# Optimization experiments

Hardware: AMD Instinct MI355X
Metric: run time of the kernel (lower is better)

## Reference

```python
import jax, jax.numpy as jnp
import numpy as np

EPS = 1e-7
TOPK = 10
IOU_THR = 0.1
REG_W, OBJ_W, CLS_W = 5.0, 1.0, 1.0
NUM_CLASSES = 80
STRIDES = (8, 16, 32)


def _corners(b):
    cx, cy, w, h = b[..., 0], b[..., 1], b[..., 2], b[..., 3]
    return cx - w / 2, cy - h / 2, cx + w / 2, cy + h / 2


def bbox_iou(box1, box2, ciou=False):
    # boxes in (cx, cy, w, h); broadcastable shapes [..., 4]
    x11, y11, x12, y12 = _corners(box1)
    x21, y21, x22, y22 = _corners(box2)
    iw = jnp.clip(jnp.minimum(x12, x22) - jnp.maximum(x11, x21), 0)
    ih = jnp.clip(jnp.minimum(y12, y22) - jnp.maximum(y11, y21), 0)
    inter = iw * ih
    a1 = (x12 - x11) * (y12 - y11)
    a2 = (x22 - x21) * (y22 - y21)
    union = a1 + a2 - inter + EPS
    iou = inter / union
    if not ciou:
        return iou
    cw = jnp.maximum(x12, x22) - jnp.minimum(x11, x21)
    ch = jnp.maximum(y12, y22) - jnp.minimum(y11, y21)
    c2 = cw ** 2 + ch ** 2 + EPS
    rho2 = ((x21 + x22 - x11 - x12) ** 2 + (y21 + y22 - y11 - y12) ** 2) / 4
    v = 4 / 3.14159 ** 2 * (jnp.arctan((x22 - x21) / (y22 - y21 + EPS))
                            - jnp.arctan((x12 - x11) / (y12 - y11 + EPS))) ** 2
    alpha = jax.lax.stop_gradient(v / (1 - iou + v + EPS))
    return iou - (rho2 / c2 + v * alpha)


def _bce_logits(x, t):
    # BCEWithLogitsLoss, reduction='none' (numerically stable)
    return jnp.maximum(x, 0) - x * t + jnp.log1p(jnp.exp(-jnp.abs(x)))


def _flat(p):
    # [B, C, H, W] -> [B, H*W, C] matching permute(1,2,0).reshape(-1, C)
    B, C, H, W = p.shape
    return p.transpose(0, 2, 3, 1).reshape(B, H * W, C)


def _grids(shapes):
    gs, ss = [], []
    for (H, W), s in zip(shapes, STRIDES):
        yv, xv = jnp.meshgrid(jnp.arange(H), jnp.arange(W), indexing='ij')
        gs.append(jnp.stack([xv, yv], -1).astype(jnp.float32).reshape(-1, 2))
        ss.append(jnp.full((H * W,), float(s), dtype=jnp.float32))
    return jnp.concatenate(gs, 0), jnp.concatenate(ss, 0)


def _yolox_loss(p3_cls, p3_reg, p3_obj, p4_cls, p4_reg, p4_obj,
                p5_cls, p5_reg, p5_obj, targets):
    B = p3_cls.shape[0]
    shapes = [p3_cls.shape[2:], p4_cls.shape[2:], p5_cls.shape[2:]]
    grids, strides = _grids(shapes)            # [A,2], [A]
    cls_preds = jnp.concatenate([_flat(p3_cls), _flat(p4_cls), _flat(p5_cls)], 1)  # [B,A,C]
    reg_preds = jnp.concatenate([_flat(p3_reg), _flat(p4_reg), _flat(p5_reg)], 1)  # [B,A,4]
    obj_preds = jnp.concatenate([_flat(p3_obj), _flat(p4_obj), _flat(p5_obj)], 1)[..., 0]  # [B,A]
    A = cls_preds.shape[1]

    # decode predicted boxes (cx, cy, w, h) in image coords
    pred_cx = (grids[:, 0] + jax.nn.sigmoid(reg_preds[..., 0])) * strides
    pred_cy = (grids[:, 1] + jax.nn.sigmoid(reg_preds[..., 1])) * strides
    pred_w = jnp.exp(reg_preds[..., 2]) * strides
    pred_h = jnp.exp(reg_preds[..., 3]) * strides
    pred_boxes = jnp.stack([pred_cx, pred_cy, pred_w, pred_h], -1)  # [B,A,4]

    # targets: (x, y, w, h, class) with x,y top-left -> center format
    t_cx = targets[..., 0] + targets[..., 2] / 2
    t_cy = targets[..., 1] + targets[..., 3] / 2
    tboxes = jnp.stack([t_cx, t_cy, targets[..., 2], targets[..., 3]], -1)  # [B,T,4]
    tcls = targets[..., 4].astype(jnp.int32)  # [B,T]

    # SimOTA-style candidate selection: top-k closest anchor centers per target
    ac = grids * strides[:, None] + strides[:, None] / 2  # [A,2]
    dist = jnp.sqrt((ac[None, None, :, 0] - t_cx[..., None]) ** 2
                    + (ac[None, None, :, 1] - t_cy[..., None]) ** 2)  # [B,T,A]
    _, idx = jax.lax.top_k(-dist, TOPK)  # [B,T,K] smallest distances

    bidx = jnp.arange(B)[:, None, None]
    sel_boxes = pred_boxes[bidx, idx]                           # [B,T,K,4]
    ious = bbox_iou(sel_boxes, tboxes[:, :, None, :])           # [B,T,K]
    valid = ious > IOU_THR
    has_valid = valid.any(-1, keepdims=True)
    fallback = jnp.arange(TOPK) == jnp.argmax(ious, -1)[..., None]
    amask = jnp.where(has_valid, valid, fallback)               # [B,T,K] bool
    w = amask.astype(jnp.float32)
    num_pos = jnp.maximum(w.sum(), 1.0)

    cious = bbox_iou(sel_boxes, tboxes[:, :, None, :], ciou=True)
    reg_sum = ((1.0 - cious) * w).sum()

    # classification loss at assigned anchors
    sel_cls = cls_preds[bidx, idx]                              # [B,T,K,C]
    onehot = jax.nn.one_hot(tcls, NUM_CLASSES, dtype=jnp.float32)[:, :, None, :]
    cls_sum = (_bce_logits(sel_cls, onehot).sum(-1) * w).sum()

    # objectness: target 1 at any assigned anchor (scatter-max), 0 elsewhere
    obj_t = jnp.zeros((B, A), jnp.float32).at[bidx, idx].max(w)
    obj_sum = _bce_logits(obj_preds, obj_t).sum()

    reg_l = reg_sum / num_pos
    obj_l = obj_sum / num_pos
    cls_l = cls_sum / num_pos
    total = REG_W * reg_l + OBJ_W * obj_l + CLS_W * cls_l
    return jnp.stack([total, reg_l, obj_l, cls_l])


def setup_inputs() -> dict:
    key = jax.random.key(0)
    ks = jax.random.split(key, 12)
    B, T = 32, 50
    d = {}
    shapes = {'p3': (80, 80), 'p4': (40, 40), 'p5': (20, 20)}
    i = 0
    for name, (H, W) in shapes.items():
        d[f'{name}_cls'] = jax.random.normal(ks[i], (B, NUM_CLASSES, H, W), jnp.float32); i += 1
        d[f'{name}_reg'] = jax.random.normal(ks[i], (B, 4, H, W), jnp.float32); i += 1
        d[f'{name}_obj'] = jax.random.normal(ks[i], (B, 1, H, W), jnp.float32); i += 1
    xy = jax.random.uniform(ks[9], (B, T, 2)) * 500.0
    wh = jax.random.uniform(ks[10], (B, T, 2)) * 120.0 + 8.0
    cls_id = jax.random.randint(ks[11], (B, T, 1), 0, NUM_CLASSES).astype(jnp.float32)
    d['targets'] = jnp.concatenate([xy, wh, cls_id], -1)
    return d


def reference(p3_cls, p3_reg, p3_obj, p4_cls, p4_reg, p4_obj,
              p5_cls, p5_reg, p5_obj, targets):
    return _yolox_loss(p3_cls, p3_reg, p3_obj, p4_cls, p4_reg, p4_obj,
                       p5_cls, p5_reg, p5_obj, targets)
```

## Files before the change

### kernel.cpp

```cpp
#include <hip/hip_runtime.h>
#include <math.h>

#define B 32
#define T 50
#define KK 10
#define NC 80
#define A_TOT 8400
#define EPSF 1e-7f
#define IOU_THR 0.1f

#define WORDS_PER_B 264
#define BITS_BYTES (B * WORDS_PER_B * 4)

__device__ __forceinline__ float softplus_bce0(float x) {
    return fmaxf(x, 0.0f) + log1pf(expf(-fabsf(x)));
}

__device__ __forceinline__ void decode_level(int a, int& aa, int& W, int& HW, float& s) {
    if (a < 6400)      { aa = a;        W = 80; HW = 6400; s = 8.0f;  }
    else if (a < 8000) { aa = a - 6400; W = 40; HW = 1600; s = 16.0f; }
    else               { aa = a - 8000; W = 20; HW = 400;  s = 32.0f; }
}

__device__ __forceinline__ unsigned long long pack_key(float d, int id) {
    return ((unsigned long long)__float_as_uint(d) << 32) | (unsigned int)id;
}

__device__ __forceinline__ void cswk(unsigned long long& ka, unsigned long long& kb) {
    if (kb < ka) { unsigned long long t = ka; ka = kb; kb = t; }
}

__global__ __launch_bounds__(64) void fused_kernel(
    const float* __restrict__ c3, const float* __restrict__ r3,
    const float* __restrict__ c4, const float* __restrict__ r4,
    const float* __restrict__ c5, const float* __restrict__ r5,
    const float* __restrict__ o3, const float* __restrict__ o4,
    const float* __restrict__ o5, const float* __restrict__ targets,
    unsigned int* __restrict__ bits, float4* __restrict__ partials)
{
    int bt = blockIdx.x;
    int b = bt / T;
    int lane = threadIdx.x;

    int gt = bt * 64 + lane;
    float ov0 = o3[gt];
    float ov1 = o3[gt + 102400];
    float ov2 = (gt < 51200) ? o4[gt] : 0.0f;
    float ov3 = (gt < 12800) ? o5[gt] : 0.0f;

    const float* tg = targets + bt * 5;
    float tw = tg[2], th = tg[3];
    float tcx = tg[0] + tw * 0.5f, tcy = tg[1] + th * 0.5f;
    int tcls = (int)tg[4];

    int ci = lane & 7, ri = lane >> 3;

    unsigned long long k0, k1, k2;
    {
        int j0 = (int)(tcx * 0.125f), i0 = (int)(tcy * 0.125f);
        int js = min(max(j0 - 3, 0), 72), is = min(max(i0 - 3, 0), 72);
        int j = js + ci, i = is + ri;
        float dx = j * 8.0f + 4.0f - tcx, dy = i * 8.0f + 4.0f - tcy;
        k0 = pack_key(sqrtf(dx * dx + dy * dy), i * 80 + j);
    }
    {
        int j0 = (int)(tcx * 0.0625f), i0 = (int)(tcy * 0.0625f);
        int js = min(max(j0 - 3, 0), 32), is = min(max(i0 - 3, 0), 32);
        int j = js + ci, i = is + ri;
        float dx = j * 16.0f + 8.0f - tcx, dy = i * 16.0f + 8.0f - tcy;
        k1 = pack_key(sqrtf(dx * dx + dy * dy), 6400 + i * 40 + j);
    }
    {
        int j0 = (int)(tcx * 0.03125f), i0 = (int)(tcy * 0.03125f);
        int js = min(max(j0 - 3, 0), 12), is = min(max(i0 - 3, 0), 12);
        int j = js + ci, i = is + ri;
        float dx = j * 32.0f + 16.0f - tcx, dy = i * 32.0f + 16.0f - tcy;
        k2 = pack_key(sqrtf(dx * dx + dy * dy), 8000 + i * 20 + j);
    }
    cswk(k0, k1); cswk(k1, k2); cswk(k0, k1);

    int a = 0;
    for (int k = 0; k < KK; ++k) {
        unsigned long long bk = k0;
#pragma unroll
        for (int sft = 1; sft < 64; sft <<= 1) {
            unsigned long long ok = __shfl_xor(bk, sft);
            if (ok < bk) bk = ok;
        }
        if (k0 == bk) {
            k0 = k1; k1 = k2; k2 = ~0ull;
        }
        if (lane == k) a = (int)(unsigned int)(bk & 0xffffffffull);
    }

    float x21 = tcx - tw * 0.5f, y21 = tcy - th * 0.5f;
    float x22 = tcx + tw * 0.5f, y22 = tcy + th * 0.5f;

    float iou = -INFINITY, ciou = 0.0f;
    bool valid = false;
    if (lane < KK) {
        int aa, W, HW; float s;
        decode_level(a, aa, W, HW, s);
        int i = aa / W, j = aa - i * W;
        const float* rb = (HW == 6400) ? r3 : (HW == 1600 ? r4 : r5);
        size_t rbase = ((size_t)b * 4) * (size_t)HW + (size_t)aa;
        float r0 = rb[rbase];
        float r1 = rb[rbase + (size_t)HW];
        float r2 = rb[rbase + 2 * (size_t)HW];
        float r3v = rb[rbase + 3 * (size_t)HW];
        float px = ((float)j + 1.0f / (1.0f + expf(-r0))) * s;
        float py = ((float)i + 1.0f / (1.0f + expf(-r1))) * s;
        float pw = expf(r2) * s;
        float ph = expf(r3v) * s;
        float x11 = px - pw * 0.5f, y11 = py - ph * 0.5f;
        float x12 = px + pw * 0.5f, y12 = py + ph * 0.5f;
        float iw = fmaxf(fminf(x12, x22) - fmaxf(x11, x21), 0.0f);
        float ih = fmaxf(fminf(y12, y22) - fmaxf(y11, y21), 0.0f);
        float inter = iw * ih;
        float a1 = (x12 - x11) * (y12 - y11);
        float a2 = (x22 - x21) * (y22 - y21);
        float uni = a1 + a2 - inter + EPSF;
        iou = inter / uni;
        valid = iou > IOU_THR;
        float cw = fmaxf(x12, x22) - fminf(x11, x21);
        float ch = fmaxf(y12, y22) - fminf(y11, y21);
        float c2 = cw * cw + ch * ch + EPSF;
        float ddx = x21 + x22 - x11 - x12;
        float ddy = y21 + y22 - y11 - y12;
        float rho2 = (ddx * ddx + ddy * ddy) * 0.25f;
        const float CPI = (float)(4.0 / (3.14159 * 3.14159));
        float dat = atanf((x22 - x21) / (y22 - y21 + EPSF))
                  - atanf((x12 - x11) / (y12 - y11 + EPSF));
        float v = CPI * dat * dat;
        float alpha = v / (1.0f - iou + v + EPSF);
        ciou = iou - (rho2 / c2 + v * alpha);
    }

    unsigned long long vmask = __ballot(valid);
    bool has_valid = (vmask != 0ull);

    float bi = iou; int bl = lane;
#pragma unroll
    for (int sft = 1; sft < 64; sft <<= 1) {
        float oi = __shfl_xor(bi, sft);
        int ol  = __shfl_xor(bl, sft);
        if (oi > bi || (oi == bi && ol < bl)) { bi = oi; bl = ol; }
    }

    bool w = (lane < KK) && (has_valid ? valid : (lane == bl));
    unsigned long long wmask0 = __ballot(w);
    int nw = __popcll(wmask0);

    float regc = w ? (1.0f - ciou) : 0.0f;
#pragma unroll
    for (int sft = 1; sft < 64; sft <<= 1) regc += __shfl_xor(regc, sft);

    unsigned int oldbits = 0, bit = 0;
    if (w) {
        bit = 1u << (a & 31);
        oldbits = atomicOr(&bits[b * WORDS_PER_B + (a >> 5)], bit);
    }

    __shared__ int s_aid[16];
    if (w) {
        int rank = __popcll(wmask0 & ((1ull << lane) - 1ull));
        s_aid[rank] = a;
    }
    __syncthreads();
    int n_items = nw * NC;

    auto cls_ptr = [&](int item, int& c) -> const float* {
        int k = item / NC;
        c = item - k * NC;
        int ak = s_aid[k];
        int aak, Wk, HWk; float sk;
        decode_level(ak, aak, Wk, HWk, sk);
        const float* cb = (HWk == 6400) ? c3 : (HWk == 1600 ? c4 : c5);
        return cb + ((size_t)b * NC + (size_t)c) * (size_t)HWk + (size_t)aak;
    };

    bool m0 = lane < n_items;
    bool m1 = 64 + lane < n_items;
    bool m2 = 128 + lane < n_items;
    bool m3 = 192 + lane < n_items;
    int cc0 = 0, cc1 = 0, cc2 = 0, cc3 = 0;
    float v0 = 0.0f, v1 = 0.0f, v2 = 0.0f, v3 = 0.0f;
    if (m0) v0 = *cls_ptr(lane, cc0);
    if (m1) v1 = *cls_ptr(64 + lane, cc1);
    if (m2) v2 = *cls_ptr(128 + lane, cc2);
    if (m3) v3 = *cls_ptr(192 + lane, cc3);

    float osum = softplus_bce0(ov0) + softplus_bce0(ov1);
    if (gt < 51200) osum += softplus_bce0(ov2);
    if (gt < 12800) osum += softplus_bce0(ov3);
    if (w && !(oldbits & bit)) {
        int aa, W, HW; float s;
        decode_level(a, aa, W, HW, s);
        const float* ob = (HW == 6400) ? o3 : (HW == 1600 ? o4 : o5);
        osum -= ob[(size_t)b * HW + aa];
    }
#pragma unroll
    for (int sft = 1; sft < 64; sft <<= 1) osum += __shfl_xor(osum, sft);

    float csum = 0.0f;
    if (m0) csum += softplus_bce0(v0) - (cc0 == tcls ? v0 : 0.0f);
    if (m1) csum += softplus_bce0(v1) - (cc1 == tcls ? v1 : 0.0f);
    if (m2) csum += softplus_bce0(v2) - (cc2 == tcls ? v2 : 0.0f);
    if (m3) csum += softplus_bce0(v3) - (cc3 == tcls ? v3 : 0.0f);
    for (int base = 256; base < n_items; base += 64) {
        int item = base + lane;
        if (item < n_items) {
            int c;
            float v = *cls_ptr(item, c);
            csum += softplus_bce0(v) - (c == tcls ? v : 0.0f);
        }
    }
#pragma unroll
    for (int sft = 1; sft < 64; sft <<= 1) csum += __shfl_xor(csum, sft);

    if (lane == 0)
        partials[bt] = make_float4(regc, csum, (float)nw, osum);
}

__global__ __launch_bounds__(256) void finalize_kernel(
    const float4* __restrict__ partials, float* __restrict__ out)
{
    int tid = threadIdx.x;
    float reg = 0.0f, cls = 0.0f, np = 0.0f, obj = 0.0f;
    for (int i = tid; i < B * T; i += 256) {
        float4 p = partials[i];
        reg += p.x; cls += p.y; np += p.z; obj += p.w;
    }
#pragma unroll
    for (int sft = 1; sft < 64; sft <<= 1) {
        reg += __shfl_xor(reg, sft);
        cls += __shfl_xor(cls, sft);
        np  += __shfl_xor(np, sft);
        obj += __shfl_xor(obj, sft);
    }
    __shared__ float sred[4][4];
    int wv = tid >> 6;
    if ((tid & 63) == 0) {
        sred[wv][0] = reg; sred[wv][1] = cls; sred[wv][2] = np; sred[wv][3] = obj;
    }
    __syncthreads();
    if (tid == 0) {
        float R = 0, C = 0, N = 0, O = 0;
        for (int i = 0; i < 4; ++i) {
            R += sred[i][0]; C += sred[i][1]; N += sred[i][2]; O += sred[i][3];
        }
        float npf = fmaxf(N, 1.0f);
        float reg_l = R / npf, cls_l = C / npf, obj_l = O / npf;
        out[0] = 5.0f * reg_l + obj_l + cls_l;
        out[1] = reg_l;
        out[2] = obj_l;
        out[3] = cls_l;
    }
}

extern "C" void kernel_launch(void* const* d_in, const int* in_sizes, int n_in,
                              void* d_out, int out_size, void* d_ws, size_t ws_size,
                              hipStream_t stream) {
    const float* p3c = (const float*)d_in[0];
    const float* p3r = (const float*)d_in[1];
    const float* p3o = (const float*)d_in[2];
    const float* p4c = (const float*)d_in[3];
    const float* p4r = (const float*)d_in[4];
    const float* p4o = (const float*)d_in[5];
    const float* p5c = (const float*)d_in[6];
    const float* p5r = (const float*)d_in[7];
    const float* p5o = (const float*)d_in[8];
    const float* targets = (const float*)d_in[9];

    char* ws = (char*)d_ws;
    unsigned int* bits = (unsigned int*)ws;
    float4* partials = (float4*)(ws + BITS_BYTES);

    hipMemsetAsync(bits, 0, BITS_BYTES, stream);

    fused_kernel<<<B * T, 64, 0, stream>>>(p3c, p3r, p4c, p4r, p5c, p5r,
                                           p3o, p4o, p5o, targets,
                                           bits, partials);
    finalize_kernel<<<1, 256, 0, stream>>>(partials, (float*)d_out);
}
```

Measured before the change: 133.5 us.

## Fuse finalize into main kernel via last-block ticket; use fast exp/log

Removes the separate finalize kernel launch: each block publishes its partial sums with release stores and bumps an atomic ticket, and the last block to arrive reduces all partials and writes the output. The ticket is zeroed by the existing memset, which now covers it. Also swaps expf/log1pf for the __expf/__logf intrinsics and moves the objectness load for each assigned anchor earlier, next to the regression loads, so its latency overlaps. This saves one kernel launch and gap at the cost of slight precision loss from the intrinsics and a serialized tail reduction done by one wave.

```diff
diff --git a/kernel.cpp b/kernel.cpp
--- a/kernel.cpp
+++ b/kernel.cpp
@@ -11,9 +11,10 @@
 
 #define WORDS_PER_B 264
 #define BITS_BYTES (B * WORDS_PER_B * 4)
+#define ZERO_BYTES (16 + BITS_BYTES)
 
 __device__ __forceinline__ float softplus_bce0(float x) {
-    return fmaxf(x, 0.0f) + log1pf(expf(-fabsf(x)));
+    return fmaxf(x, 0.0f) + __logf(1.0f + __expf(-fabsf(x)));
 }
 
 __device__ __forceinline__ void decode_level(int a, int& aa, int& W, int& HW, float& s) {
@@ -36,7 +37,8 @@
     const float* __restrict__ c5, const float* __restrict__ r5,
     const float* __restrict__ o3, const float* __restrict__ o4,
     const float* __restrict__ o5, const float* __restrict__ targets,
-    unsigned int* __restrict__ bits, float4* __restrict__ partials)
+    unsigned int* __restrict__ ticket, unsigned int* __restrict__ bits,
+    float* __restrict__ partials, float* __restrict__ out)
 {
     int bt = blockIdx.x;
     int b = bt / T;
@@ -96,22 +98,24 @@
     float x21 = tcx - tw * 0.5f, y21 = tcy - th * 0.5f;
     float x22 = tcx + tw * 0.5f, y22 = tcy + th * 0.5f;
 
-    float iou = -INFINITY, ciou = 0.0f;
+    float iou = -INFINITY, ciou = 0.0f, ospec = 0.0f;
     bool valid = false;
     if (lane < KK) {
         int aa, W, HW; float s;
         decode_level(a, aa, W, HW, s);
         int i = aa / W, j = aa - i * W;
         const float* rb = (HW == 6400) ? r3 : (HW == 1600 ? r4 : r5);
+        const float* ob = (HW == 6400) ? o3 : (HW == 1600 ? o4 : o5);
         size_t rbase = ((size_t)b * 4) * (size_t)HW + (size_t)aa;
         float r0 = rb[rbase];
         float r1 = rb[rbase + (size_t)HW];
         float r2 = rb[rbase + 2 * (size_t)HW];
         float r3v = rb[rbase + 3 * (size_t)HW];
-        float px = ((float)j + 1.0f / (1.0f + expf(-r0))) * s;
-        float py = ((float)i + 1.0f / (1.0f + expf(-r1))) * s;
-        float pw = expf(r2) * s;
-        float ph = expf(r3v) * s;
+        ospec = ob[(size_t)b * HW + aa];
+        float px = ((float)j + 1.0f / (1.0f + __expf(-r0))) * s;
+        float py = ((float)i + 1.0f / (1.0f + __expf(-r1))) * s;
+        float pw = __expf(r2) * s;
+        float ph = __expf(r3v) * s;
         float x11 = px - pw * 0.5f, y11 = py - ph * 0.5f;
         float x12 = px + pw * 0.5f, y12 = py + ph * 0.5f;
         float iw = fmaxf(fminf(x12, x22) - fmaxf(x11, x21), 0.0f);
@@ -193,12 +197,7 @@
     float osum = softplus_bce0(ov0) + softplus_bce0(ov1);
     if (gt < 51200) osum += softplus_bce0(ov2);
     if (gt < 12800) osum += softplus_bce0(ov3);
-    if (w && !(oldbits & bit)) {
-        int aa, W, HW; float s;
-        decode_level(a, aa, W, HW, s);
-        const float* ob = (HW == 6400) ? o3 : (HW == 1600 ? o4 : o5);
-        osum -= ob[(size_t)b * HW + aa];
-    }
+    if (w && !(oldbits & bit)) osum -= ospec;
 #pragma unroll
     for (int sft = 1; sft < 64; sft <<= 1) osum += __shfl_xor(osum, sft);
 
@@ -218,43 +217,40 @@
 #pragma unroll
     for (int sft = 1; sft < 64; sft <<= 1) csum += __shfl_xor(csum, sft);
 
-    if (lane == 0)
-        partials[bt] = make_float4(regc, csum, (float)nw, osum);
-}
-
-__global__ __launch_bounds__(256) void finalize_kernel(
-    const float4* __restrict__ partials, float* __restrict__ out)
-{
-    int tid = threadIdx.x;
-    float reg = 0.0f, cls = 0.0f, np = 0.0f, obj = 0.0f;
-    for (int i = tid; i < B * T; i += 256) {
-        float4 p = partials[i];
-        reg += p.x; cls += p.y; np += p.z; obj += p.w;
-    }
-#pragma unroll
-    for (int sft = 1; sft < 64; sft <<= 1) {
-        reg += __shfl_xor(reg, sft);
-        cls += __shfl_xor(cls, sft);
-        np  += __shfl_xor(np, sft);
-        obj += __shfl_xor(obj, sft);
-    }
-    __shared__ float sred[4][4];
-    int wv = tid >> 6;
-    if ((tid & 63) == 0) {
-        sred[wv][0] = reg; sred[wv][1] = cls; sred[wv][2] = np; sred[wv][3] = obj;
-    }
-    __syncthreads();
-    if (tid == 0) {
-        float R = 0, C = 0, N = 0, O = 0;
-        for (int i = 0; i < 4; ++i) {
-            R += sred[i][0]; C += sred[i][1]; N += sred[i][2]; O += sred[i][3];
-        }
-        float npf = fmaxf(N, 1.0f);
-        float reg_l = R / npf, cls_l = C / npf, obj_l = O / npf;
-        out[0] = 5.0f * reg_l + obj_l + cls_l;
-        out[1] = reg_l;
-        out[2] = obj_l;
-        out[3] = cls_l;
+    unsigned int t = 0;
+    if (lane == 0) {
+        float* pf = partials + bt * 4;
+        __hip_atomic_store(pf + 0, regc, __ATOMIC_RELEASE, __HIP_MEMORY_SCOPE_AGENT);
+        __hip_atomic_store(pf + 1, csum, __ATOMIC_RELEASE, __HIP_MEMORY_SCOPE_AGENT);
+        __hip_atomic_store(pf + 2, (float)nw, __ATOMIC_RELEASE, __HIP_MEMORY_SCOPE_AGENT);
+        __hip_atomic_store(pf + 3, osum, __ATOMIC_RELEASE, __HIP_MEMORY_SCOPE_AGENT);
+        t = __hip_atomic_fetch_add(ticket, 1u, __ATOMIC_ACQ_REL, __HIP_MEMORY_SCOPE_AGENT);
+    }
+    t = __shfl(t, 0);
+    if (t == (unsigned int)(B * T - 1)) {
+        float reg = 0.0f, cls = 0.0f, np = 0.0f, obj = 0.0f;
+        for (int i = lane; i < B * T; i += 64) {
+            const float* q = partials + i * 4;
+            reg += __hip_atomic_load(q + 0, __ATOMIC_ACQUIRE, __HIP_MEMORY_SCOPE_AGENT);
+            cls += __hip_atomic_load(q + 1, __ATOMIC_ACQUIRE, __HIP_MEMORY_SCOPE_AGENT);
+            np  += __hip_atomic_load(q + 2, __ATOMIC_ACQUIRE, __HIP_MEMORY_SCOPE_AGENT);
+            obj += __hip_atomic_load(q + 3, __ATOMIC_ACQUIRE, __HIP_MEMORY_SCOPE_AGENT);
+        }
+#pragma unroll
+        for (int sft = 1; sft < 64; sft <<= 1) {
+            reg += __shfl_xor(reg, sft);
+            cls += __shfl_xor(cls, sft);
+            np  += __shfl_xor(np, sft);
+            obj += __shfl_xor(obj, sft);
+        }
+        if (lane == 0) {
+            float npf = fmaxf(np, 1.0f);
+            float reg_l = reg / npf, cls_l = cls / npf, obj_l = obj / npf;
+            out[0] = 5.0f * reg_l + obj_l + cls_l;
+            out[1] = reg_l;
+            out[2] = obj_l;
+            out[3] = cls_l;
+        }
     }
 }
 
@@ -273,13 +269,14 @@
     const float* targets = (const float*)d_in[9];
 
     char* ws = (char*)d_ws;
-    unsigned int* bits = (unsigned int*)ws;
-    float4* partials = (float4*)(ws + BITS_BYTES);
-
-    hipMemsetAsync(bits, 0, BITS_BYTES, stream);
+    unsigned int* ticket = (unsigned int*)ws;
+    unsigned int* bits = (unsigned int*)(ws + 16);
+    float* partials = (float*)(ws + ZERO_BYTES);
+
+    hipMemsetAsync(d_ws, 0, ZERO_BYTES, stream);
 
     fused_kernel<<<B * T, 64, 0, stream>>>(p3c, p3r, p4c, p4r, p5c, p5r,
                                            p3o, p4o, p5o, targets,
-                                           bits, partials);
-    finalize_kernel<<<1, 256, 0, stream>>>(partials, (float*)d_out);
-}
+                                           ticket, bits, partials,
+                                           (float*)d_out);
+}
```

New measurement: 252.5 us. +89.1%, slower.
